# Performance work log

Measured on AMD Instinct MI355X. Metric: run time of the kernel, lower is better.

## Reference

```python
import jax, jax.numpy as jnp
import numpy as np

NUM_USER = 100000
NUM_ITEM = 50000
DIM = 64
NUM_EDGES = 3200000


def setup_inputs() -> dict:
    key = jax.random.key(0)
    k1, k2, k3, k4 = jax.random.split(key, 4)
    return {
        "user_embedding": jax.random.normal(k1, (NUM_USER, DIM), dtype=jnp.float32),
        "item_embedding": jax.random.normal(k2, (NUM_ITEM, DIM), dtype=jnp.float32),
        "edge_user": jax.random.randint(k3, (NUM_EDGES,), 0, NUM_USER, dtype=jnp.int32).astype(jnp.int64),
        "edge_item": jax.random.randint(k4, (NUM_EDGES,), 0, NUM_ITEM, dtype=jnp.int32).astype(jnp.int64),
    }


def _segment_mean(feats, idx, num_segments):
    # scatter_mean semantics: sum per segment / count, empty segments -> 0
    s = jax.ops.segment_sum(feats, idx, num_segments=num_segments)  # [n, dim]
    cnt = jax.ops.segment_sum(jnp.ones((idx.shape[0], 1), feats.dtype), idx,
                              num_segments=num_segments)  # [n, 1]
    return s / jnp.maximum(cnt, 1.0)


def reference(user_embedding, item_embedding, edge_user, edge_item):
    num_user = user_embedding.shape[0]
    num_item = item_embedding.shape[0]

    # view1: aggregate_neighbor_features — mean of purchased-item embeddings per user
    neighbor_feat = _segment_mean(item_embedding[edge_item], edge_user, num_user)

    # view2: aggregate_cooccurrence_features — two-stage mean aggregation
    # stage 1: per item, mean of its purchasers' embeddings
    item_user_agg = _segment_mean(user_embedding[edge_user], edge_item, num_item)
    # stage 2: per user, mean of stage-1 features of purchased items
    cooccur_feat = _segment_mean(item_user_agg[edge_item], edge_user, num_user)

    return (neighbor_feat, cooccur_feat)
```

## Files before the change

### kernel.cpp

```cpp
#include <hip/hip_runtime.h>
#include <hip/hip_fp16.h>

constexpr int NUM_USER  = 100000;
constexpr int NUM_ITEM  = 50000;
constexpr int DIM       = 64;
constexpr int NUM_EDGES = 3200000;

constexpr int KPB   = 32;
constexpr int NB_U  = (NUM_USER + KPB - 1) / KPB;
constexpr int NB_I  = (NUM_ITEM + KPB - 1) / KPB;
constexpr int CHUNK = 4096;
constexpr int CSH   = 14;
constexpr int NCH_I = 4;
constexpr int NCH_U = 7;
constexpr int CAP_U = 1280;
constexpr int CAP_I = 2304;

__device__ __forceinline__ __half2 u2h(unsigned u) {
  union { unsigned u; __half2 h; } v; v.u = u; return v.h;
}
__device__ __forceinline__ unsigned h2u(__half2 h) {
  union { __half2 h; unsigned u; } v; v.h = h; return v.u;
}

__device__ __forceinline__ int detect64(const void* eu, const void* ei) {
  const int* a = (const int*)eu;
  const int* b = (const int*)ei;
  int any = 0;
#pragma unroll
  for (int i = 1; i < 64; i += 2) { any |= a[i]; any |= b[i]; }
  return any == 0;
}

__device__ __forceinline__ int idx_at(const void* p, int e, int is64) {
  return is64 ? ((const int*)p)[2 * e] : ((const int*)p)[e];
}

__global__ void k_cvt(const float* __restrict__ ue, unsigned* __restrict__ u32,
                      const float* __restrict__ ie, unsigned* __restrict__ fused) {
  const int nu = NUM_USER * 32, ni = NUM_ITEM * 32;
  for (int t = blockIdx.x * blockDim.x + threadIdx.x; t < nu + ni;
       t += gridDim.x * blockDim.x) {
    if (t < nu) {
      const float2 v = ((const float2*)ue)[t];
      u32[t] = h2u(__floats2half2_rn(v.x, v.y));
    } else {
      const int s = t - nu;
      const float2 v = ((const float2*)ie)[s];
      fused[(size_t)(s >> 5) * 64 + 2 * (s & 31)] = h2u(__floats2half2_rn(v.x, v.y));
    }
  }
}

__global__ void k_part2(const void* eu_p, const void* ei_p,
                        int* gcur_i, unsigned int* __restrict__ pairs_i,
                        int* gcur_u, unsigned int* __restrict__ pairs_u,
                        int capI, int capU) {
  __shared__ int hist_u[NB_U], base_u[NB_U];
  __shared__ int hist_i[NB_I], base_i[NB_I];
  for (int t = threadIdx.x; t < NB_U; t += blockDim.x) hist_u[t] = 0;
  for (int t = threadIdx.x; t < NB_I; t += blockDim.x) hist_i[t] = 0;
  __syncthreads();
  const int is64 = detect64(eu_p, ei_p);
  const int ch = NUM_EDGES / gridDim.x;
  const int lo = blockIdx.x * ch, hiE = lo + ch;
  for (int e = lo + threadIdx.x; e < hiE; e += blockDim.x) {
    atomicAdd(&hist_u[idx_at(eu_p, e, is64) >> 5], 1);
    atomicAdd(&hist_i[idx_at(ei_p, e, is64) >> 5], 1);
  }
  __syncthreads();
  for (int t = threadIdx.x; t < NB_U; t += blockDim.x) {
    const int h = hist_u[t];
    int b = 0;
    if (h) {
      b = atomicAdd(&gcur_u[t], h);
      if (capU) b += t * capU;
    }
    base_u[t] = b;
    hist_u[t] = 0;
  }
  for (int t = threadIdx.x; t < NB_I; t += blockDim.x) {
    const int h = hist_i[t];
    int b = 0;
    if (h) {
      b = atomicAdd(&gcur_i[t], h);
      if (capI) b += t * capI;
    }
    base_i[t] = b;
    hist_i[t] = 0;
  }
  __syncthreads();
  for (int e = lo + threadIdx.x; e < hiE; e += blockDim.x) {
    const int eu = idx_at(eu_p, e, is64);
    const int ei = idx_at(ei_p, e, is64);
    const int bi = ei >> 5;
    const int pi = base_i[bi] + atomicAdd(&hist_i[bi], 1);
    if (!capI || pi < (bi + 1) * capI)
      pairs_i[pi] = ((unsigned)(ei & 31) << 17) | (unsigned)eu;
    const int bu = eu >> 5;
    const int pu = base_u[bu] + atomicAdd(&hist_u[bu], 1);
    if (!capU || pu < (bu + 1) * capU)
      pairs_u[pu] = ((unsigned)(eu & 31) << 17) | (unsigned)ei;
  }
}

__global__ void k_hist_part(const void* eu_p, const void* ei_p,
                            int* __restrict__ partials) {
  __shared__ int hu[NB_U];
  __shared__ int hi_[NB_I];
  for (int t = threadIdx.x; t < NB_U; t += blockDim.x) hu[t] = 0;
  for (int t = threadIdx.x; t < NB_I; t += blockDim.x) hi_[t] = 0;
  __syncthreads();
  const int is64 = detect64(eu_p, ei_p);
  const int ga = gridDim.x;
  const int ch = NUM_EDGES / ga;
  const int b = blockIdx.x;
  const int lo = b * ch, hiE = lo + ch;
  for (int e = lo + threadIdx.x; e < hiE; e += blockDim.x) {
    atomicAdd(&hu[idx_at(eu_p, e, is64) >> 5], 1);
    atomicAdd(&hi_[idx_at(ei_p, e, is64) >> 5], 1);
  }
  __syncthreads();
  int* pu = partials;
  int* pi = partials + (size_t)NB_U * ga;
  for (int t = threadIdx.x; t < NB_U; t += blockDim.x) pu[(size_t)t * ga + b] = hu[t];
  for (int t = threadIdx.x; t < NB_I; t += blockDim.x) pi[(size_t)t * ga + b] = hi_[t];
}

__global__ void k_hist_reduce(const int* __restrict__ partials, int ga,
                              int* __restrict__ gcnt_u, int* __restrict__ gcnt_i) {
  const int k = blockIdx.x * blockDim.x + threadIdx.x;
  if (k >= NB_U + NB_I) return;
  const int* base = (k < NB_U) ? partials + (size_t)k * ga
                               : partials + (size_t)NB_U * ga + (size_t)(k - NB_U) * ga;
  int s = 0;
  for (int b = 0; b < ga; ++b) s += base[b];
  if (k < NB_U) gcnt_u[k] = s;
  else          gcnt_i[k - NB_U] = s;
}

__device__ void scan_body(const int* __restrict__ in, int* __restrict__ out,
                          int* __restrict__ cur, int n) {
  __shared__ int part[1024];
  const int t = threadIdx.x;
  const int chunk = (n + 1023) >> 10;
  const int lo = min(t * chunk, n);
  const int hi = min(lo + chunk, n);
  int s = 0;
  for (int i = lo; i < hi; ++i) s += in[i];
  part[t] = s;
  __syncthreads();
  for (int d = 1; d < 1024; d <<= 1) {
    int v = (t >= d) ? part[t - d] : 0;
    __syncthreads();
    part[t] += v;
    __syncthreads();
  }
  int run = (t == 0) ? 0 : part[t - 1];
  for (int i = lo; i < hi; ++i) {
    int v = in[i];
    out[i] = run; cur[i] = run; run += v;
  }
  if (t == 1023) out[n] = part[1023];
}

__global__ void k_scan2(const int* cu, int* bu, int* curu,
                        const int* ci, int* bi, int* curi) {
  if (blockIdx.x == 0) scan_body(cu, bu, curu, NB_U);
  else                 scan_body(ci, bi, curi, NB_I);
}

__device__ __forceinline__ void bucket_extent(int bucket, const int* gbase,
                                              const int* gcnt, int cap,
                                              int& lo, int& hi) {
  if (cap > 0) {
    lo = bucket * cap;
    hi = lo + min(gcnt[bucket], cap);
  } else {
    lo = gbase[bucket];
    hi = gbase[bucket + 1];
  }
}

__global__ __launch_bounds__(256, 8)
void k_agg_item(const unsigned* __restrict__ user32,
                const unsigned int* __restrict__ pairs,
                const int* __restrict__ gbase, const int* __restrict__ gcnt,
                int cap, unsigned* __restrict__ fused) {
  constexpr int NBINS = NCH_U * KPB;
  __shared__ int sorted[CHUNK];
  __shared__ int hist[NBINS], base[NBINS], cur[NBINS];
  __shared__ int gsum[NCH_U];
  const int tid = threadIdx.x;
  const int lane = tid & 63;
  const int wid = tid >> 6;
  const int half = lane >> 5;
  const int c = lane & 31;
  const int bucket = blockIdx.x;
  int lo, hi;
  bucket_extent(bucket, gbase, gcnt, cap, lo, hi);

  unsigned s[8]; int cnt[8];
#pragma unroll
  for (int r = 0; r < 8; ++r) { s[r] = 0u; cnt[r] = 0; }

  for (int clo = lo; clo < hi; clo += CHUNK) {
    const int csz = min(CHUNK, hi - clo);
    for (int t = tid; t < NBINS; t += 256) hist[t] = 0;
    __syncthreads();
    for (int j = tid; j < csz; j += 256) {
      const unsigned p = pairs[clo + j];
      atomicAdd(&hist[((p & 0x1FFFF) >> CSH) * KPB + (p >> 17)], 1);
    }
    __syncthreads();
    if (tid < NCH_U) {
      int g = 0;
      for (int q = 0; q < KPB; ++q) g += hist[tid * KPB + q];
      gsum[tid] = g;
    }
    __syncthreads();
    for (int t = tid; t < NBINS; t += 256) {
      const int ch = t >> 5;
      int b = 0;
      for (int q = 0; q < ch; ++q) b += gsum[q];
      for (int q = ch * KPB; q < t; ++q) b += hist[q];
      base[t] = b; cur[t] = b;
    }
    __syncthreads();
    for (int j = tid; j < csz; j += 256) {
      const unsigned p = pairs[clo + j];
      const int v = (int)(p & 0x1FFFF);
      const int slot = atomicAdd(&cur[(v >> CSH) * KPB + (p >> 17)], 1);
      sorted[slot] = v;
    }
    __syncthreads();
    for (int ch = 0; ch < NCH_U; ++ch) {
#pragma unroll
      for (int r = 0; r < 8; ++r) {
        const int bin = ch * KPB + wid * 8 + r;
        const int jlo = base[bin], jhi = cur[bin];
        cnt[r] += jhi - jlo;
        for (int j = jlo; j < jhi; j += 8) {
          unsigned w[4];
#pragma unroll
          for (int q = 0; q < 4; ++q) {
            const int jj = j + 2 * q + half;
            w[q] = (jj < jhi) ? user32[(size_t)sorted[jj] * 32 + c] : 0u;
          }
#pragma unroll
          for (int q = 0; q < 4; ++q)
            s[r] = h2u(__hadd2(u2h(s[r]), u2h(w[q])));
        }
      }
    }
    __syncthreads();
  }

  const int i0 = bucket * KPB;
#pragma unroll
  for (int r = 0; r < 8; ++r) {
    const unsigned o = (unsigned)__shfl_xor((int)s[r], 32);
    const __half2 tot = __hadd2(u2h(s[r]), u2h(o));
    const int item = i0 + wid * 8 + r;
    if (half == 0 && item < NUM_ITEM) {
      const float inv = 1.0f / fmaxf((float)cnt[r], 1.f);
      fused[(size_t)item * 64 + 2 * c + 1] =
          h2u(__floats2half2_rn(__low2float(tot) * inv, __high2float(tot) * inv));
    }
  }
}

__global__ __launch_bounds__(256, 8)
void k_agg_user(const unsigned* __restrict__ fused,
                const unsigned int* __restrict__ pairs,
                const int* __restrict__ gbase, const int* __restrict__ gcnt,
                int cap,
                float* __restrict__ out0, float* __restrict__ out1) {
  constexpr int NBINS = NCH_I * KPB;
  __shared__ int sorted[CHUNK];
  __shared__ int hist[NBINS], base[NBINS], cur[NBINS];
  __shared__ int gsum[NCH_I];
  const int tid = threadIdx.x;
  const int lane = tid & 63;
  const int wid = tid >> 6;
  const int half = lane >> 5;
  const int c = lane & 31;
  const int bucket = blockIdx.x;
  int lo, hi;
  bucket_extent(bucket, gbase, gcnt, cap, lo, hi);
  const uint2* fused2 = (const uint2*)fused;

  unsigned s0[8], s1[8]; int cnt[8];
#pragma unroll
  for (int r = 0; r < 8; ++r) { s0[r] = 0u; s1[r] = 0u; cnt[r] = 0; }

  for (int clo = lo; clo < hi; clo += CHUNK) {
    const int csz = min(CHUNK, hi - clo);
    for (int t = tid; t < NBINS; t += 256) hist[t] = 0;
    __syncthreads();
    for (int j = tid; j < csz; j += 256) {
      const unsigned p = pairs[clo + j];
      atomicAdd(&hist[((p & 0x1FFFF) >> CSH) * KPB + (p >> 17)], 1);
    }
    __syncthreads();
    if (tid < NCH_I) {
      int g = 0;
      for (int q = 0; q < KPB; ++q) g += hist[tid * KPB + q];
      gsum[tid] = g;
    }
    __syncthreads();
    for (int t = tid; t < NBINS; t += 256) {
      const int ch = t >> 5;
      int b = 0;
      for (int q = 0; q < ch; ++q) b += gsum[q];
      for (int q = ch * KPB; q < t; ++q) b += hist[q];
      base[t] = b; cur[t] = b;
    }
    __syncthreads();
    for (int j = tid; j < csz; j += 256) {
      const unsigned p = pairs[clo + j];
      const int v = (int)(p & 0x1FFFF);
      const int slot = atomicAdd(&cur[(v >> CSH) * KPB + (p >> 17)], 1);
      sorted[slot] = v;
    }
    __syncthreads();
    for (int ch = 0; ch < NCH_I; ++ch) {
#pragma unroll
      for (int r = 0; r < 8; ++r) {
        const int bin = ch * KPB + wid * 8 + r;
        const int jlo = base[bin], jhi = cur[bin];
        cnt[r] += jhi - jlo;
        for (int j = jlo; j < jhi; j += 8) {
          uint2 w[4];
#pragma unroll
          for (int q = 0; q < 4; ++q) {
            const int jj = j + 2 * q + half;
            w[q] = (jj < jhi) ? fused2[(size_t)sorted[jj] * 32 + c]
                              : make_uint2(0u, 0u);
          }
#pragma unroll
          for (int q = 0; q < 4; ++q) {
            s0[r] = h2u(__hadd2(u2h(s0[r]), u2h(w[q].x)));
            s1[r] = h2u(__hadd2(u2h(s1[r]), u2h(w[q].y)));
          }
        }
      }
    }
    __syncthreads();
  }

  const int u0 = bucket * KPB;
#pragma unroll
  for (int r = 0; r < 8; ++r) {
    const unsigned o0 = (unsigned)__shfl_xor((int)s0[r], 32);
    const unsigned o1 = (unsigned)__shfl_xor((int)s1[r], 32);
    const __half2 t0 = __hadd2(u2h(s0[r]), u2h(o0));
    const __half2 t1 = __hadd2(u2h(s1[r]), u2h(o1));
    const int u = u0 + wid * 8 + r;
    if (half == 0 && u < NUM_USER) {
      const float inv = 1.0f / fmaxf((float)cnt[r], 1.f);
      ((float2*)out0)[(size_t)u * 32 + c] =
          make_float2(__low2float(t0) * inv, __high2float(t0) * inv);
      ((float2*)out1)[(size_t)u * 32 + c] =
          make_float2(__low2float(t1) * inv, __high2float(t1) * inv);
    }
  }
}

__global__ void k_scatter1(const float* __restrict__ user_emb,
                           const float* __restrict__ item_emb,
                           const void* eu_p, const void* ei_p,
                           float* out0, float* item_sum,
                           float* cnt_user, float* cnt_item) {
  const int is64 = detect64(eu_p, ei_p);
  const int lane = threadIdx.x & (DIM - 1);
  const int sub  = threadIdx.x >> 6;
  const int epb  = blockDim.x >> 6;
  for (int e = blockIdx.x * epb + sub; e < NUM_EDGES; e += gridDim.x * epb) {
    const int eu = idx_at(eu_p, e, is64);
    const int ei = idx_at(ei_p, e, is64);
    atomicAdd(&out0[eu * DIM + lane], item_emb[ei * DIM + lane]);
    atomicAdd(&item_sum[ei * DIM + lane], user_emb[eu * DIM + lane]);
    if (lane == 0) {
      atomicAdd(&cnt_user[eu], 1.0f);
      atomicAdd(&cnt_item[ei], 1.0f);
    }
  }
}

__global__ void k_div_item(float* item_sum, const float* __restrict__ cnt_item) {
  const int n = NUM_ITEM * DIM;
  for (int t = blockIdx.x * blockDim.x + threadIdx.x; t < n;
       t += gridDim.x * blockDim.x)
    item_sum[t] /= fmaxf(cnt_item[t >> 6], 1.0f);
}

__global__ void k_scatter2(const float* __restrict__ item_agg,
                           const void* eu_p, const void* ei_p, float* out1) {
  const int is64 = detect64(eu_p, ei_p);
  const int lane = threadIdx.x & (DIM - 1);
  const int sub  = threadIdx.x >> 6;
  const int epb  = blockDim.x >> 6;
  for (int e = blockIdx.x * epb + sub; e < NUM_EDGES; e += gridDim.x * epb) {
    const int eu = idx_at(eu_p, e, is64);
    const int ei = idx_at(ei_p, e, is64);
    atomicAdd(&out1[eu * DIM + lane], item_agg[ei * DIM + lane]);
  }
}

__global__ void k_finalize(float* out0, float* out1,
                           const float* __restrict__ cnt_user) {
  const int n = NUM_USER * DIM;
  for (int t = blockIdx.x * blockDim.x + threadIdx.x; t < n;
       t += gridDim.x * blockDim.x) {
    const float c = fmaxf(cnt_user[t >> 6], 1.0f);
    out0[t] /= c;
    out1[t] /= c;
  }
}

extern "C" void kernel_launch(void* const* d_in, const int* in_sizes, int n_in,
                              void* d_out, int out_size, void* d_ws, size_t ws_size,
                              hipStream_t stream) {
  const float* user_emb = (const float*)d_in[0];
  const float* item_emb = (const float*)d_in[1];
  const void*  eu_p     = d_in[2];
  const void*  ei_p     = d_in[3];

  float* out0 = (float*)d_out;
  float* out1 = out0 + (size_t)NUM_USER * DIM;

  int* wsi = (int*)d_ws;
  float* wsf = (float*)d_ws;

  const size_t s_pairs_u = 0;
  const size_t s_pairs_i = s_pairs_u + (size_t)NB_U * CAP_U;
  const size_t s_user32  = s_pairs_i + (size_t)NB_I * CAP_I;
  const size_t s_fused   = s_user32 + (size_t)NUM_USER * 32;
  const size_t s_gcur_u  = s_fused + (size_t)NUM_ITEM * 64;
  const size_t s_gcur_i  = s_gcur_u + NB_U;
  const size_t s_end     = s_gcur_i + NB_I;
  const size_t need_static = s_end * 4;

  const size_t o_pairs   = 0;
  const size_t o_user32  = o_pairs + NUM_EDGES;
  const size_t o_fused   = o_user32 + (size_t)NUM_USER * 32;
  const size_t o_gcnt_u  = o_fused + (size_t)NUM_ITEM * 64;
  const size_t o_gbase_u = o_gcnt_u + NB_U;
  const size_t o_gcur_u  = o_gbase_u + NB_U + 1;
  const size_t o_gcnt_i  = o_gcur_u + NB_U;
  const size_t o_gbase_i = o_gcnt_i + NB_I;
  const size_t o_gcur_i  = o_gbase_i + NB_I + 1;
  const size_t o_pairs2  = o_gcur_i + NB_I;
  const size_t need_dynamic = (o_pairs2 + NUM_EDGES) * 4;

  if (ws_size >= need_static) {
    unsigned int* pairs_u = (unsigned int*)(wsi + s_pairs_u);
    unsigned int* pairs_i = (unsigned int*)(wsi + s_pairs_i);
    unsigned* user32 = (unsigned*)(wsi + s_user32);
    unsigned* fused  = (unsigned*)(wsi + s_fused);
    int* gcur_u = wsi + s_gcur_u;
    int* gcur_i = wsi + s_gcur_i;

    hipMemsetAsync(gcur_u, 0, (size_t)(NB_U + NB_I) * 4, stream);
    k_cvt<<<1536, 256, 0, stream>>>(user_emb, user32, item_emb, fused);
    k_part2<<<256, 1024, 0, stream>>>(eu_p, ei_p, gcur_i, pairs_i,
                                      gcur_u, pairs_u, CAP_I, CAP_U);
    k_agg_item<<<NB_I, 256, 0, stream>>>(user32, pairs_i, nullptr,
                                         gcur_i, CAP_I, fused);
    k_agg_user<<<NB_U, 256, 0, stream>>>(fused, pairs_u, nullptr,
                                         gcur_u, CAP_U, out0, out1);
  } else if (ws_size >= need_dynamic) {
    unsigned int* pairs_i  = (unsigned int*)(wsi + o_pairs);
    int*          partials = wsi + o_pairs;
    unsigned* user32 = (unsigned*)(wsi + o_user32);
    unsigned* fused  = (unsigned*)(wsi + o_fused);
    int* gcnt_u  = wsi + o_gcnt_u;
    int* gbase_u = wsi + o_gbase_u;
    int* gcur_u  = wsi + o_gcur_u;
    int* gcnt_i  = wsi + o_gcnt_i;
    int* gbase_i = wsi + o_gbase_i;
    int* gcur_i  = wsi + o_gcur_i;
    unsigned int* pairs_u = (unsigned int*)(wsi + o_pairs2);

    k_hist_part<<<256, 512, 0, stream>>>(eu_p, ei_p, partials);
    k_hist_reduce<<<(NB_U + NB_I + 255) / 256, 256, 0, stream>>>(partials, 256,
                                                                 gcnt_u, gcnt_i);
    k_scan2<<<2, 1024, 0, stream>>>(gcnt_u, gbase_u, gcur_u,
                                    gcnt_i, gbase_i, gcur_i);
    k_cvt<<<1536, 256, 0, stream>>>(user_emb, user32, item_emb, fused);
    k_part2<<<256, 1024, 0, stream>>>(eu_p, ei_p, gcur_i, pairs_i,
                                      gcur_u, pairs_u, 0, 0);
    k_agg_item<<<NB_I, 256, 0, stream>>>(user32, pairs_i, gbase_i,
                                         nullptr, 0, fused);
    k_agg_user<<<NB_U, 256, 0, stream>>>(fused, pairs_u, gbase_u,
                                         nullptr, 0, out0, out1);
  } else {
    float* item_sum = wsf;
    float* cnt_user = wsf + (size_t)NUM_ITEM * DIM;
    float* cnt_item = cnt_user + NUM_USER;
    const size_t used = ((size_t)NUM_ITEM * DIM + NUM_USER + NUM_ITEM) * 4;

    hipMemsetAsync(d_out, 0, (size_t)out_size * sizeof(float), stream);
    hipMemsetAsync(d_ws, 0, used, stream);
    k_scatter1<<<4096, 256, 0, stream>>>(user_emb, item_emb, eu_p, ei_p,
                                         out0, item_sum, cnt_user, cnt_item);
    k_div_item<<<2048, 256, 0, stream>>>(item_sum, cnt_item);
    k_scatter2<<<4096, 256, 0, stream>>>(item_sum, eu_p, ei_p, out1);
    k_finalize<<<2048, 256, 0, stream>>>(out0, out1, cnt_user);
  }
}
```

Before: 251.0 us.

## Fuse fp16 conversion into partition kernel via extra blocks; use nontemporal loads

The separate embedding-to-half conversion kernel is merged into the partition kernel as 64 extra blocks, so conversion runs at the same time as edge partitioning and one launch disappears. The conversion and the pair-list reads in the aggregation kernels now use nontemporal loads and stores to reduce cache pollution. The risk is that the conversion blocks reserve large static shared memory they never use, which limits occupancy, and that nontemporal hints may evict data that later kernels reuse.

```diff
diff --git a/kernel.cpp b/kernel.cpp
--- a/kernel.cpp
+++ b/kernel.cpp
@@ -15,12 +15,17 @@
 constexpr int NCH_U = 7;
 constexpr int CAP_U = 1280;
 constexpr int CAP_I = 2304;
+constexpr int PGRID = 256;
+constexpr int CVTB  = 64;
 
 __device__ __forceinline__ __half2 u2h(unsigned u) {
   union { unsigned u; __half2 h; } v; v.u = u; return v.h;
 }
 __device__ __forceinline__ unsigned h2u(__half2 h) {
   union { __half2 h; unsigned u; } v; v.h = h; return v.u;
+}
+__device__ __forceinline__ float u_as_f(unsigned u) {
+  union { unsigned u; float f; } v; v.u = u; return v.f;
 }
 
 __device__ __forceinline__ int detect64(const void* eu, const void* ei) {
@@ -36,33 +41,49 @@
   return is64 ? ((const int*)p)[2 * e] : ((const int*)p)[e];
 }
 
-__global__ void k_cvt(const float* __restrict__ ue, unsigned* __restrict__ u32,
-                      const float* __restrict__ ie, unsigned* __restrict__ fused) {
+__device__ __forceinline__ void cvt_body(int t0, int stride,
+                                         const float* __restrict__ ue,
+                                         unsigned* __restrict__ u32,
+                                         const float* __restrict__ ie,
+                                         unsigned* __restrict__ fused) {
   const int nu = NUM_USER * 32, ni = NUM_ITEM * 32;
-  for (int t = blockIdx.x * blockDim.x + threadIdx.x; t < nu + ni;
-       t += gridDim.x * blockDim.x) {
+  for (int t = t0; t < nu + ni; t += stride) {
     if (t < nu) {
-      const float2 v = ((const float2*)ue)[t];
-      u32[t] = h2u(__floats2half2_rn(v.x, v.y));
+      const unsigned long long raw =
+          __builtin_nontemporal_load((const unsigned long long*)ue + t);
+      const __half2 h = __floats2half2_rn(u_as_f((unsigned)raw),
+                                          u_as_f((unsigned)(raw >> 32)));
+      __builtin_nontemporal_store(h2u(h), &u32[t]);
     } else {
       const int s = t - nu;
-      const float2 v = ((const float2*)ie)[s];
-      fused[(size_t)(s >> 5) * 64 + 2 * (s & 31)] = h2u(__floats2half2_rn(v.x, v.y));
-    }
-  }
-}
-
-__global__ void k_part2(const void* eu_p, const void* ei_p,
-                        int* gcur_i, unsigned int* __restrict__ pairs_i,
-                        int* gcur_u, unsigned int* __restrict__ pairs_u,
-                        int capI, int capU) {
+      const unsigned long long raw =
+          __builtin_nontemporal_load((const unsigned long long*)ie + s);
+      const __half2 h = __floats2half2_rn(u_as_f((unsigned)raw),
+                                          u_as_f((unsigned)(raw >> 32)));
+      __builtin_nontemporal_store(h2u(h),
+                                  &fused[(size_t)(s >> 5) * 64 + 2 * (s & 31)]);
+    }
+  }
+}
+
+__global__ void k_part2cvt(const void* eu_p, const void* ei_p,
+                           int* gcur_i, unsigned int* __restrict__ pairs_i,
+                           int* gcur_u, unsigned int* __restrict__ pairs_u,
+                           int capI, int capU,
+                           const float* __restrict__ ue, unsigned* __restrict__ u32t,
+                           const float* __restrict__ ie, unsigned* __restrict__ fusedt) {
   __shared__ int hist_u[NB_U], base_u[NB_U];
   __shared__ int hist_i[NB_I], base_i[NB_I];
+  if (blockIdx.x >= PGRID) {
+    cvt_body((blockIdx.x - PGRID) * blockDim.x + threadIdx.x,
+             CVTB * blockDim.x, ue, u32t, ie, fusedt);
+    return;
+  }
   for (int t = threadIdx.x; t < NB_U; t += blockDim.x) hist_u[t] = 0;
   for (int t = threadIdx.x; t < NB_I; t += blockDim.x) hist_i[t] = 0;
   __syncthreads();
   const int is64 = detect64(eu_p, ei_p);
-  const int ch = NUM_EDGES / gridDim.x;
+  const int ch = NUM_EDGES / PGRID;
   const int lo = blockIdx.x * ch, hiE = lo + ch;
   for (int e = lo + threadIdx.x; e < hiE; e += blockDim.x) {
     atomicAdd(&hist_u[idx_at(eu_p, e, is64) >> 5], 1);
@@ -209,7 +230,7 @@
     for (int t = tid; t < NBINS; t += 256) hist[t] = 0;
     __syncthreads();
     for (int j = tid; j < csz; j += 256) {
-      const unsigned p = pairs[clo + j];
+      const unsigned p = __builtin_nontemporal_load(&pairs[clo + j]);
       atomicAdd(&hist[((p & 0x1FFFF) >> CSH) * KPB + (p >> 17)], 1);
     }
     __syncthreads();
@@ -228,7 +249,7 @@
     }
     __syncthreads();
     for (int j = tid; j < csz; j += 256) {
-      const unsigned p = pairs[clo + j];
+      const unsigned p = __builtin_nontemporal_load(&pairs[clo + j]);
       const int v = (int)(p & 0x1FFFF);
       const int slot = atomicAdd(&cur[(v >> CSH) * KPB + (p >> 17)], 1);
       sorted[slot] = v;
@@ -299,7 +320,7 @@
     for (int t = tid; t < NBINS; t += 256) hist[t] = 0;
     __syncthreads();
     for (int j = tid; j < csz; j += 256) {
-      const unsigned p = pairs[clo + j];
+      const unsigned p = __builtin_nontemporal_load(&pairs[clo + j]);
       atomicAdd(&hist[((p & 0x1FFFF) >> CSH) * KPB + (p >> 17)], 1);
     }
     __syncthreads();
@@ -318,7 +339,7 @@
     }
     __syncthreads();
     for (int j = tid; j < csz; j += 256) {
-      const unsigned p = pairs[clo + j];
+      const unsigned p = __builtin_nontemporal_load(&pairs[clo + j]);
       const int v = (int)(p & 0x1FFFF);
       const int slot = atomicAdd(&cur[(v >> CSH) * KPB + (p >> 17)], 1);
       sorted[slot] = v;
@@ -463,9 +484,9 @@
     int* gcur_i = wsi + s_gcur_i;
 
     hipMemsetAsync(gcur_u, 0, (size_t)(NB_U + NB_I) * 4, stream);
-    k_cvt<<<1536, 256, 0, stream>>>(user_emb, user32, item_emb, fused);
-    k_part2<<<256, 1024, 0, stream>>>(eu_p, ei_p, gcur_i, pairs_i,
-                                      gcur_u, pairs_u, CAP_I, CAP_U);
+    k_part2cvt<<<PGRID + CVTB, 1024, 0, stream>>>(
+        eu_p, ei_p, gcur_i, pairs_i, gcur_u, pairs_u, CAP_I, CAP_U,
+        user_emb, user32, item_emb, fused);
     k_agg_item<<<NB_I, 256, 0, stream>>>(user32, pairs_i, nullptr,
                                          gcur_i, CAP_I, fused);
     k_agg_user<<<NB_U, 256, 0, stream>>>(fused, pairs_u, nullptr,
@@ -488,9 +509,9 @@
                                                                  gcnt_u, gcnt_i);
     k_scan2<<<2, 1024, 0, stream>>>(gcnt_u, gbase_u, gcur_u,
                                     gcnt_i, gbase_i, gcur_i);
-    k_cvt<<<1536, 256, 0, stream>>>(user_emb, user32, item_emb, fused);
-    k_part2<<<256, 1024, 0, stream>>>(eu_p, ei_p, gcur_i, pairs_i,
-                                      gcur_u, pairs_u, 0, 0);
+    k_part2cvt<<<PGRID + CVTB, 1024, 0, stream>>>(
+        eu_p, ei_p, gcur_i, pairs_i, gcur_u, pairs_u, 0, 0,
+        user_emb, user32, item_emb, fused);
     k_agg_item<<<NB_I, 256, 0, stream>>>(user32, pairs_i, gbase_i,
                                          nullptr, 0, fused);
     k_agg_user<<<NB_U, 256, 0, stream>>>(fused, pairs_u, gbase_u,
```

Result: slower. 286.1 us (+14.0%).
